# Performance work log

Hardware: AMD Instinct MI355X
Metric: run time of the kernel (lower is better)

## Reference

```python
import jax, jax.numpy as jnp
import numpy as np

SR = 48000
N_FFT = 2048
HOP = 64
N_MELS = 128
N_FREQ = N_FFT // 2 + 1  # 1025
N_TARGETS = 64
BATCH = 32
AUDIO_LEN = SR * 1  # duration = 1 s


def _mel_filterbank():
    # torchaudio melscale_fbanks defaults: htk mel scale, norm=None, f_min=0, f_max=sr/2
    freqs = np.linspace(0.0, SR / 2.0, N_FREQ)
    h2m = lambda f: 2595.0 * np.log10(1.0 + f / 700.0)
    m2h = lambda m: 700.0 * (10.0 ** (m / 2595.0) - 1.0)
    m_pts = np.linspace(h2m(0.0), h2m(SR / 2.0), N_MELS + 2)
    f_pts = m2h(m_pts)
    f_diff = np.diff(f_pts)
    slopes = f_pts[None, :] - freqs[:, None]          # [F, n_mels+2]
    down = -slopes[:, :-2] / f_diff[:-1]
    up = slopes[:, 2:] / f_diff[1:]
    fb = np.maximum(0.0, np.minimum(down, up))        # [F, n_mels]
    return fb.astype(np.float32)


def _mel_spec(x, fb):
    # x: [B, L] raw audio -> [B, n_mels, T] power mel spectrogram (power=2, center=True, hann)
    pad = N_FFT // 2
    xp = jnp.pad(x, ((0, 0), (pad, pad)), mode='reflect')
    n_frames = 1 + x.shape[-1] // HOP                 # 751
    idx = jnp.arange(n_frames)[:, None] * HOP + jnp.arange(N_FFT)[None, :]
    frames = xp[:, idx]                               # [B, T, n_fft]
    win = (0.5 * (1.0 - jnp.cos(2.0 * jnp.pi * jnp.arange(N_FFT) / N_FFT))).astype(x.dtype)
    spec = jnp.fft.rfft(frames * win, axis=-1)        # [B, T, F]
    power = spec.real ** 2 + spec.imag ** 2
    return jnp.einsum('btf,fm->bmt', power, fb)       # [B, n_mels, T]


def setup_inputs() -> dict:
    key = jax.random.key(0)
    k1, k2 = jax.random.split(key)
    fb = jnp.asarray(_mel_filterbank())
    x = jax.random.normal(k1, (BATCH, AUDIO_LEN), dtype=jnp.float32) * 0.1
    target_audio = jax.random.normal(k2, (N_TARGETS, AUDIO_LEN), dtype=jnp.float32) * 0.1
    mel_targets = _mel_spec(target_audio, fb)         # [N, n_mels, T]
    return {"x": x, "mel_targets": mel_targets, "mel_fb": fb}


def reference(x, mel_targets, mel_fb):
    m = _mel_spec(x, mel_fb)                          # [B, n_mels, T]
    # mean abs diff of each candidate vs every target: [B, N]
    diffs = jnp.mean(jnp.abs(m[:, None, :, :] - mel_targets[None, :, :, :]), axis=(-1, -2))
    minimums = jnp.min(diffs, axis=-1)                # [B]
    return (minimums,)
```

## Files before the change

### kernel.cpp

```cpp
#include <hip/hip_runtime.h>
#include <math.h>

#define SRATE   48000
#define NFFT    2048
#define N1      1024
#define HOP     64
#define NMELS   128
#define NFREQ   1025
#define NTGT    64
#define BATCH   32
#define NFRAMES 751
#define MELSZ   (NMELS * NFRAMES)
#define NCHUNK  751
#define CPB     1
#define NB_B    ((NCHUNK + CPB - 1) / CPB)
#define PADW    132

__device__ __forceinline__ int SP(int a) { return a + 5 * (a >> 5); }
#define SBUF1 1179
__device__ __forceinline__ int TP(int a) { return a + (a >> 5); }
#define TWP   263

__global__ __launch_bounds__(256) void tab_kernel(
    float* __restrict__ wtab, float* __restrict__ gtwc, float* __restrict__ gtws) {
  int i = blockIdx.x * 256 + threadIdx.x;
  if (i < NFFT)
    wtab[i] = 0.5f - 0.5f * cosf((float)(2.0 * M_PI / NFFT) * (float)i);
  if (i <= 1024) {
    float sv, cv;
    sincosf(-(float)(2.0 * M_PI / NFFT) * (float)i, &sv, &cv);
    gtwc[i] = cv;
    gtws[i] = sv;
  }
}

__global__ __launch_bounds__(256) void fbt_kernel(
    const float* __restrict__ fb, float* __restrict__ fbT,
    int* __restrict__ fs, int* __restrict__ fe) {
  int m = blockIdx.x;
  int tid = threadIdx.x;
  __shared__ int smin[256], smax[256];
  int lmin = NFREQ, lmax = -1;
  for (int f = tid; f < NFREQ; f += 256) {
    float v = fb[f * NMELS + m];
    fbT[m * NFREQ + f] = v;
    if (v > 0.0f) {
      if (f < lmin) lmin = f;
      if (f > lmax) lmax = f;
    }
  }
  smin[tid] = lmin;
  smax[tid] = lmax;
  __syncthreads();
  for (int off = 128; off > 0; off >>= 1) {
    if (tid < off) {
      smin[tid] = min(smin[tid], smin[tid + off]);
      smax[tid] = max(smax[tid], smax[tid + off]);
    }
    __syncthreads();
  }
  if (tid == 0) {
    fs[m] = smin[0];
    fe[m] = smax[0];
  }
}

template<int L>
__device__ __forceinline__ void r4_1024(
    const float* __restrict__ sre, const float* __restrict__ sim,
    float* __restrict__ dre, float* __restrict__ dim_,
    const float* __restrict__ twc, const float* __restrict__ tws, int t) {
  constexpr int LOG2L = (L == 1) ? 0 : (L == 4) ? 2 : (L == 16) ? 4
                      : (L == 64) ? 6 : 8;
  constexpr int TS = 256 / L;
  int k = t & (L - 1);
  int j = t >> LOG2L;
  int rb = SP(t);
  float u0r = sre[rb],       u0i = sim[rb];
  float u1r = sre[rb + 296], u1i = sim[rb + 296];
  float u2r = sre[rb + 592], u2i = sim[rb + 592];
  float u3r = sre[rb + 888], u3i = sim[rb + 888];
  float a1r, a1i, a2r, a2i, a3r, a3i;
  if (L == 1) {
    a1r = u1r; a1i = u1i; a2r = u2r; a2i = u2i; a3r = u3r; a3i = u3i;
  } else {
    int tp = TP(k * TS);
    float wc1 = twc[tp], ws1 = tws[tp];
    float wc2 = wc1 * wc1 - ws1 * ws1, ws2 = 2.0f * wc1 * ws1;
    float wc3 = wc2 * wc1 - ws2 * ws1, ws3 = wc2 * ws1 + ws2 * wc1;
    a1r = wc1 * u1r - ws1 * u1i; a1i = wc1 * u1i + ws1 * u1r;
    a2r = wc2 * u2r - ws2 * u2i; a2i = wc2 * u2i + ws2 * u2r;
    a3r = wc3 * u3r - ws3 * u3i; a3i = wc3 * u3i + ws3 * u3r;
  }
  float s0r = u0r + a2r, s0i = u0i + a2i;
  float d0r = u0r - a2r, d0i = u0i - a2i;
  float s1r = a1r + a3r, s1i = a1i + a3i;
  float d1r = a1r - a3r, d1i = a1i - a3i;
  int wb = (j << (LOG2L + 2)) + k;
  int o0 = SP(wb), o1 = SP(wb + L), o2 = SP(wb + 2 * L), o3 = SP(wb + 3 * L);
  dre[o0] = s0r + s1r;  dim_[o0] = s0i + s1i;
  dre[o1] = d0r + d1i;  dim_[o1] = d0i - d1r;
  dre[o2] = s0r - s1r;  dim_[o2] = s0i - s1i;
  dre[o3] = d0r - d1i;  dim_[o3] = d0i + d1r;
}

__global__ __launch_bounds__(256) void melspec_kernel(
    const float* __restrict__ x, const float* __restrict__ fbT,
    const int* __restrict__ fs, const int* __restrict__ fe,
    const float* __restrict__ wtab, const float* __restrict__ gtwc,
    const float* __restrict__ gtws, float* __restrict__ mel) {
  __shared__ float lds[4 * SBUF1 + 2 * TWP];
  float* reA  = lds;
  float* imA  = lds + SBUF1;
  float* reB  = lds + 2 * SBUF1;
  float* imB  = lds + 3 * SBUF1;
  float* tw1c = lds + 4 * SBUF1;
  float* tw1s = lds + 4 * SBUF1 + TWP;

  int tid = threadIdx.x;
  int b = blockIdx.x / NFRAMES;
  int t = blockIdx.x - b * NFRAMES;
  const float* xb = x + (size_t)b * SRATE;

  {
    int j = tid;
    tw1c[TP(j)] = gtwc[2 * j];
    tw1s[TP(j)] = gtws[2 * j];
  }
  for (int n = tid; n < N1; n += 256) {
    int i0 = 2 * n, i1 = 2 * n + 1;
    int p0 = t * HOP + i0 - NFFT / 2;
    p0 = p0 < 0 ? -p0 : (p0 >= SRATE ? 2 * SRATE - 2 - p0 : p0);
    int p1 = t * HOP + i1 - NFFT / 2;
    p1 = p1 < 0 ? -p1 : (p1 >= SRATE ? 2 * SRATE - 2 - p1 : p1);
    int s = SP(n);
    reA[s] = xb[p0] * wtab[i0];
    imA[s] = xb[p1] * wtab[i1];
  }
  __syncthreads();

  r4_1024<1>(reA, imA, reB, imB, tw1c, tw1s, tid);   __syncthreads();
  r4_1024<4>(reB, imB, reA, imA, tw1c, tw1s, tid);   __syncthreads();
  r4_1024<16>(reA, imA, reB, imB, tw1c, tw1s, tid);  __syncthreads();
  r4_1024<64>(reB, imB, reA, imA, tw1c, tw1s, tid);  __syncthreads();
  r4_1024<256>(reA, imA, reB, imB, tw1c, tw1s, tid); __syncthreads();

  for (int k = tid; k <= 1024; k += 256) {
    int ka = SP(k & (N1 - 1)), kb = SP((N1 - k) & (N1 - 1));
    float Zar = reB[ka], Zai = imB[ka];
    float Zbr = reB[kb], Zbi = imB[kb];
    float Xer  = 0.5f * (Zar + Zbr), Xei = 0.5f * (Zai - Zbi);
    float Xor_ = 0.5f * (Zai + Zbi), Xoi = 0.5f * (Zbr - Zar);
    float wc = gtwc[k], ws = gtws[k];
    float Xr = Xer + wc * Xor_ - ws * Xoi;
    float Xi = Xei + wc * Xoi + ws * Xor_;
    reA[k] = Xr * Xr + Xi * Xi;
  }
  __syncthreads();

  int m = tid >> 1, half = tid & 1;
  int f0 = fs[m], f1 = fe[m];
  int mid = f0 + ((f1 - f0 + 1) >> 1);
  int lo = half ? mid : f0;
  int hi = half ? f1 : mid - 1;
  const float* col = fbT + (size_t)m * NFREQ;
  float acc = 0.0f;
  for (int f = lo; f <= hi; ++f) acc += reA[f] * col[f];
  acc += __shfl_xor(acc, 1);
  if (!half) mel[(size_t)b * MELSZ + m * NFRAMES + t] = acc;
}

__global__ __launch_bounds__(256) void diff_kernel(
    const float* __restrict__ mel, const float* __restrict__ tgt,
    float* __restrict__ part) {
  __shared__ float mel_s[BATCH * PADW];
  __shared__ float tgt_s[NTGT * PADW];
  int tid = threadIdx.x;
  int b = tid >> 3;
  int kb = tid & 7;

  float acc[8];
  #pragma unroll
  for (int i = 0; i < 8; ++i) acc[i] = 0.0f;

  for (int cc = 0; cc < CPB; ++cc) {
    int c = blockIdx.x * CPB + cc;
    if (c >= NCHUNK) break;
    __syncthreads();
    for (int q = tid; q < BATCH * 32; q += 256) {
      int row = q >> 5, c4 = q & 31;
      float4 v = *(const float4*)(mel + (size_t)row * MELSZ + c * 128 + c4 * 4);
      *(float4*)(&mel_s[row * PADW + c4 * 4]) = v;
    }
    for (int q = tid; q < NTGT * 32; q += 256) {
      int row = q >> 5, c4 = q & 31;
      float4 v = *(const float4*)(tgt + (size_t)row * MELSZ + c * 128 + c4 * 4);
      *(float4*)(&tgt_s[row * PADW + c4 * 4]) = v;
    }
    __syncthreads();
    for (int j4 = 0; j4 < 32; ++j4) {
      float4 mv = *(const float4*)(&mel_s[b * PADW + j4 * 4]);
      #pragma unroll
      for (int i = 0; i < 8; ++i) {
        int k = kb + (i << 3);
        float4 tv = *(const float4*)(&tgt_s[k * PADW + j4 * 4]);
        acc[i] += fabsf(mv.x - tv.x) + fabsf(mv.y - tv.y) +
                  fabsf(mv.z - tv.z) + fabsf(mv.w - tv.w);
      }
    }
  }

  #pragma unroll
  for (int i = 0; i < 8; ++i)
    part[(size_t)blockIdx.x * 2048 + b * 64 + kb + (i << 3)] = acc[i];
}

__global__ __launch_bounds__(256) void reduce_kernel(
    const float* __restrict__ part, float* __restrict__ out) {
  __shared__ float ds[256];
  int tid = threadIdx.x;
  int p = blockIdx.x * 256 + tid;
  float s = 0.0f;
  for (int bb = 0; bb < NB_B; ++bb) s += part[(size_t)bb * 2048 + p];
  ds[tid] = s * (1.0f / (float)MELSZ);
  __syncthreads();
  if (tid < 4) {
    float mn = ds[tid * 64];
    #pragma unroll
    for (int kk = 1; kk < 64; ++kk) mn = fminf(mn, ds[tid * 64 + kk]);
    out[blockIdx.x * 4 + tid] = mn;
  }
}

extern "C" void kernel_launch(void* const* d_in, const int* in_sizes, int n_in,
                              void* d_out, int out_size, void* d_ws, size_t ws_size,
                              hipStream_t stream) {
  const float* x   = (const float*)d_in[0];
  const float* tgt = (const float*)d_in[1];
  const float* fb  = (const float*)d_in[2];
  float* out = (float*)d_out;

  char* ws = (char*)d_ws;
  size_t off = 0;
  float* fbT = (float*)(ws + off);
  off += ((size_t)NMELS * NFREQ * sizeof(float) + 255) & ~(size_t)255;
  int* fs = (int*)(ws + off); off += 1024;
  int* fe = (int*)(ws + off); off += 1024;
  float* wtab = (float*)(ws + off); off += NFFT * sizeof(float);
  float* gtwc = (float*)(ws + off); off += 1056 * sizeof(float);
  float* gtws = (float*)(ws + off); off += 1056 * sizeof(float);
  float* mel = (float*)(ws + off);
  off += (size_t)BATCH * MELSZ * sizeof(float);
  float* part = (float*)(ws + off);
  off += (size_t)NB_B * 2048 * sizeof(float);

  tab_kernel<<<8, 256, 0, stream>>>(wtab, gtwc, gtws);
  fbt_kernel<<<NMELS, 256, 0, stream>>>(fb, fbT, fs, fe);
  melspec_kernel<<<BATCH * NFRAMES, 256, 0, stream>>>(
      x, fbT, fs, fe, wtab, gtwc, gtws, mel);
  diff_kernel<<<NB_B, 256, 0, stream>>>(mel, tgt, part);
  reduce_kernel<<<8, 256, 0, stream>>>(part, out);
}
```

Baseline: 291.3 us.

## Interleave complex FFT data as float2, vectorize frame loads, atomically reduce diffs

The FFT workspace in LDS moves from split real/imag arrays to interleaved float2, and the window and twiddle tables become float2, so each butterfly reads and writes complex values with single 64-bit LDS accesses. Interior frame samples are loaded as float2 from global memory, with the reflect-padding path kept only at the edges. The diff kernel computes a 2x4 register tile per thread and atomically adds into a single 2048-entry buffer. This removes the per-chunk partial buffer and the long serial sum in the reduce kernel, at the cost of many float atomics, a memset launch, and order-dependent float summation.

New measurement: 241.4 us. 17.1% less time.

```diff
diff --git a/kernel.cpp b/kernel.cpp
--- a/kernel.cpp
+++ b/kernel.cpp
@@ -12,8 +12,6 @@
 #define NFRAMES 751
 #define MELSZ   (NMELS * NFRAMES)
 #define NCHUNK  751
-#define CPB     1
-#define NB_B    ((NCHUNK + CPB - 1) / CPB)
 #define PADW    132
 
 __device__ __forceinline__ int SP(int a) { return a + 5 * (a >> 5); }
@@ -22,15 +20,17 @@
 #define TWP   263
 
 __global__ __launch_bounds__(256) void tab_kernel(
-    float* __restrict__ wtab, float* __restrict__ gtwc, float* __restrict__ gtws) {
+    float2* __restrict__ wtab2, float2* __restrict__ gtw) {
   int i = blockIdx.x * 256 + threadIdx.x;
-  if (i < NFFT)
-    wtab[i] = 0.5f - 0.5f * cosf((float)(2.0 * M_PI / NFFT) * (float)i);
+  if (i < N1) {
+    float w0 = 0.5f - 0.5f * cosf((float)(2.0 * M_PI / NFFT) * (float)(2 * i));
+    float w1 = 0.5f - 0.5f * cosf((float)(2.0 * M_PI / NFFT) * (float)(2 * i + 1));
+    wtab2[i] = make_float2(w0, w1);
+  }
   if (i <= 1024) {
     float sv, cv;
     sincosf(-(float)(2.0 * M_PI / NFFT) * (float)i, &sv, &cv);
-    gtwc[i] = cv;
-    gtws[i] = sv;
+    gtw[i] = make_float2(cv, sv);
   }
 }
 
@@ -67,94 +67,87 @@
 
 template<int L>
 __device__ __forceinline__ void r4_1024(
-    const float* __restrict__ sre, const float* __restrict__ sim,
-    float* __restrict__ dre, float* __restrict__ dim_,
-    const float* __restrict__ twc, const float* __restrict__ tws, int t) {
+    const float2* __restrict__ s, float2* __restrict__ d,
+    const float2* __restrict__ tw, int t) {
   constexpr int LOG2L = (L == 1) ? 0 : (L == 4) ? 2 : (L == 16) ? 4
                       : (L == 64) ? 6 : 8;
   constexpr int TS = 256 / L;
   int k = t & (L - 1);
   int j = t >> LOG2L;
   int rb = SP(t);
-  float u0r = sre[rb],       u0i = sim[rb];
-  float u1r = sre[rb + 296], u1i = sim[rb + 296];
-  float u2r = sre[rb + 592], u2i = sim[rb + 592];
-  float u3r = sre[rb + 888], u3i = sim[rb + 888];
+  float2 u0 = s[rb], u1 = s[rb + 296], u2 = s[rb + 592], u3 = s[rb + 888];
   float a1r, a1i, a2r, a2i, a3r, a3i;
   if (L == 1) {
-    a1r = u1r; a1i = u1i; a2r = u2r; a2i = u2i; a3r = u3r; a3i = u3i;
+    a1r = u1.x; a1i = u1.y; a2r = u2.x; a2i = u2.y; a3r = u3.x; a3i = u3.y;
   } else {
-    int tp = TP(k * TS);
-    float wc1 = twc[tp], ws1 = tws[tp];
+    float2 w = tw[TP(k * TS)];
+    float wc1 = w.x, ws1 = w.y;
     float wc2 = wc1 * wc1 - ws1 * ws1, ws2 = 2.0f * wc1 * ws1;
     float wc3 = wc2 * wc1 - ws2 * ws1, ws3 = wc2 * ws1 + ws2 * wc1;
-    a1r = wc1 * u1r - ws1 * u1i; a1i = wc1 * u1i + ws1 * u1r;
-    a2r = wc2 * u2r - ws2 * u2i; a2i = wc2 * u2i + ws2 * u2r;
-    a3r = wc3 * u3r - ws3 * u3i; a3i = wc3 * u3i + ws3 * u3r;
-  }
-  float s0r = u0r + a2r, s0i = u0i + a2i;
-  float d0r = u0r - a2r, d0i = u0i - a2i;
+    a1r = wc1 * u1.x - ws1 * u1.y; a1i = wc1 * u1.y + ws1 * u1.x;
+    a2r = wc2 * u2.x - ws2 * u2.y; a2i = wc2 * u2.y + ws2 * u2.x;
+    a3r = wc3 * u3.x - ws3 * u3.y; a3i = wc3 * u3.y + ws3 * u3.x;
+  }
+  float s0r = u0.x + a2r, s0i = u0.y + a2i;
+  float d0r = u0.x - a2r, d0i = u0.y - a2i;
   float s1r = a1r + a3r, s1i = a1i + a3i;
   float d1r = a1r - a3r, d1i = a1i - a3i;
   int wb = (j << (LOG2L + 2)) + k;
-  int o0 = SP(wb), o1 = SP(wb + L), o2 = SP(wb + 2 * L), o3 = SP(wb + 3 * L);
-  dre[o0] = s0r + s1r;  dim_[o0] = s0i + s1i;
-  dre[o1] = d0r + d1i;  dim_[o1] = d0i - d1r;
-  dre[o2] = s0r - s1r;  dim_[o2] = s0i - s1i;
-  dre[o3] = d0r - d1i;  dim_[o3] = d0i + d1r;
+  d[SP(wb)]         = make_float2(s0r + s1r, s0i + s1i);
+  d[SP(wb + L)]     = make_float2(d0r + d1i, d0i - d1r);
+  d[SP(wb + 2 * L)] = make_float2(s0r - s1r, s0i - s1i);
+  d[SP(wb + 3 * L)] = make_float2(d0r - d1i, d0i + d1r);
 }
 
 __global__ __launch_bounds__(256) void melspec_kernel(
     const float* __restrict__ x, const float* __restrict__ fbT,
     const int* __restrict__ fs, const int* __restrict__ fe,
-    const float* __restrict__ wtab, const float* __restrict__ gtwc,
-    const float* __restrict__ gtws, float* __restrict__ mel) {
-  __shared__ float lds[4 * SBUF1 + 2 * TWP];
-  float* reA  = lds;
-  float* imA  = lds + SBUF1;
-  float* reB  = lds + 2 * SBUF1;
-  float* imB  = lds + 3 * SBUF1;
-  float* tw1c = lds + 4 * SBUF1;
-  float* tw1s = lds + 4 * SBUF1 + TWP;
+    const float2* __restrict__ wtab2, const float2* __restrict__ gtw,
+    float* __restrict__ mel) {
+  __shared__ float2 zA[SBUF1];
+  __shared__ float2 zB[SBUF1];
+  __shared__ float2 twl[TWP];
 
   int tid = threadIdx.x;
   int b = blockIdx.x / NFRAMES;
   int t = blockIdx.x - b * NFRAMES;
   const float* xb = x + (size_t)b * SRATE;
 
-  {
-    int j = tid;
-    tw1c[TP(j)] = gtwc[2 * j];
-    tw1s[TP(j)] = gtws[2 * j];
-  }
+  twl[TP(tid)] = gtw[2 * tid];
+
+  int base = t * HOP - NFFT / 2;
   for (int n = tid; n < N1; n += 256) {
-    int i0 = 2 * n, i1 = 2 * n + 1;
-    int p0 = t * HOP + i0 - NFFT / 2;
-    p0 = p0 < 0 ? -p0 : (p0 >= SRATE ? 2 * SRATE - 2 - p0 : p0);
-    int p1 = t * HOP + i1 - NFFT / 2;
-    p1 = p1 < 0 ? -p1 : (p1 >= SRATE ? 2 * SRATE - 2 - p1 : p1);
-    int s = SP(n);
-    reA[s] = xb[p0] * wtab[i0];
-    imA[s] = xb[p1] * wtab[i1];
-  }
-  __syncthreads();
-
-  r4_1024<1>(reA, imA, reB, imB, tw1c, tw1s, tid);   __syncthreads();
-  r4_1024<4>(reB, imB, reA, imA, tw1c, tw1s, tid);   __syncthreads();
-  r4_1024<16>(reA, imA, reB, imB, tw1c, tw1s, tid);  __syncthreads();
-  r4_1024<64>(reB, imB, reA, imA, tw1c, tw1s, tid);  __syncthreads();
-  r4_1024<256>(reA, imA, reB, imB, tw1c, tw1s, tid); __syncthreads();
-
+    int p0 = base + 2 * n;
+    float2 v;
+    if (p0 >= 0 && p0 + 1 < SRATE) {
+      v = *(const float2*)(xb + p0);
+    } else {
+      int q0 = p0 < 0 ? -p0 : (p0 >= SRATE ? 2 * SRATE - 2 - p0 : p0);
+      int p1 = p0 + 1;
+      int q1 = p1 < 0 ? -p1 : (p1 >= SRATE ? 2 * SRATE - 2 - p1 : p1);
+      v = make_float2(xb[q0], xb[q1]);
+    }
+    float2 w2 = wtab2[n];
+    zA[SP(n)] = make_float2(v.x * w2.x, v.y * w2.y);
+  }
+  __syncthreads();
+
+  r4_1024<1>(zA, zB, twl, tid);   __syncthreads();
+  r4_1024<4>(zB, zA, twl, tid);   __syncthreads();
+  r4_1024<16>(zA, zB, twl, tid);  __syncthreads();
+  r4_1024<64>(zB, zA, twl, tid);  __syncthreads();
+  r4_1024<256>(zA, zB, twl, tid); __syncthreads();
+
+  float* pw = (float*)zA;
   for (int k = tid; k <= 1024; k += 256) {
     int ka = SP(k & (N1 - 1)), kb = SP((N1 - k) & (N1 - 1));
-    float Zar = reB[ka], Zai = imB[ka];
-    float Zbr = reB[kb], Zbi = imB[kb];
-    float Xer  = 0.5f * (Zar + Zbr), Xei = 0.5f * (Zai - Zbi);
-    float Xor_ = 0.5f * (Zai + Zbi), Xoi = 0.5f * (Zbr - Zar);
-    float wc = gtwc[k], ws = gtws[k];
-    float Xr = Xer + wc * Xor_ - ws * Xoi;
-    float Xi = Xei + wc * Xoi + ws * Xor_;
-    reA[k] = Xr * Xr + Xi * Xi;
+    float2 Za = zB[ka], Zb = zB[kb];
+    float Xer  = 0.5f * (Za.x + Zb.x), Xei = 0.5f * (Za.y - Zb.y);
+    float Xor_ = 0.5f * (Za.y + Zb.y), Xoi = 0.5f * (Zb.x - Za.x);
+    float2 w = gtw[k];
+    float Xr = Xer + w.x * Xor_ - w.y * Xoi;
+    float Xi = Xei + w.x * Xoi + w.y * Xor_;
+    pw[k] = Xr * Xr + Xi * Xi;
   }
   __syncthreads();
 
@@ -165,64 +158,66 @@
   int hi = half ? f1 : mid - 1;
   const float* col = fbT + (size_t)m * NFREQ;
   float acc = 0.0f;
-  for (int f = lo; f <= hi; ++f) acc += reA[f] * col[f];
+  for (int f = lo; f <= hi; ++f) acc += pw[f] * col[f];
   acc += __shfl_xor(acc, 1);
   if (!half) mel[(size_t)b * MELSZ + m * NFRAMES + t] = acc;
 }
 
 __global__ __launch_bounds__(256) void diff_kernel(
     const float* __restrict__ mel, const float* __restrict__ tgt,
-    float* __restrict__ part) {
+    float* __restrict__ diffs) {
   __shared__ float mel_s[BATCH * PADW];
   __shared__ float tgt_s[NTGT * PADW];
   int tid = threadIdx.x;
-  int b = tid >> 3;
-  int kb = tid & 7;
-
-  float acc[8];
+  int bg = tid >> 4;
+  int kg = tid & 15;
+  int c = blockIdx.x;
+
+  for (int q = tid; q < BATCH * 32; q += 256) {
+    int row = q >> 5, c4 = q & 31;
+    float4 v = *(const float4*)(mel + (size_t)row * MELSZ + c * 128 + c4 * 4);
+    *(float4*)(&mel_s[row * PADW + c4 * 4]) = v;
+  }
+  for (int q = tid; q < NTGT * 32; q += 256) {
+    int row = q >> 5, c4 = q & 31;
+    float4 v = *(const float4*)(tgt + (size_t)row * MELSZ + c * 128 + c4 * 4);
+    *(float4*)(&tgt_s[row * PADW + c4 * 4]) = v;
+  }
+  __syncthreads();
+
+  float acc[2][4];
   #pragma unroll
-  for (int i = 0; i < 8; ++i) acc[i] = 0.0f;
-
-  for (int cc = 0; cc < CPB; ++cc) {
-    int c = blockIdx.x * CPB + cc;
-    if (c >= NCHUNK) break;
-    __syncthreads();
-    for (int q = tid; q < BATCH * 32; q += 256) {
-      int row = q >> 5, c4 = q & 31;
-      float4 v = *(const float4*)(mel + (size_t)row * MELSZ + c * 128 + c4 * 4);
-      *(float4*)(&mel_s[row * PADW + c4 * 4]) = v;
-    }
-    for (int q = tid; q < NTGT * 32; q += 256) {
-      int row = q >> 5, c4 = q & 31;
-      float4 v = *(const float4*)(tgt + (size_t)row * MELSZ + c * 128 + c4 * 4);
-      *(float4*)(&tgt_s[row * PADW + c4 * 4]) = v;
-    }
-    __syncthreads();
-    for (int j4 = 0; j4 < 32; ++j4) {
-      float4 mv = *(const float4*)(&mel_s[b * PADW + j4 * 4]);
-      #pragma unroll
-      for (int i = 0; i < 8; ++i) {
-        int k = kb + (i << 3);
-        float4 tv = *(const float4*)(&tgt_s[k * PADW + j4 * 4]);
-        acc[i] += fabsf(mv.x - tv.x) + fabsf(mv.y - tv.y) +
-                  fabsf(mv.z - tv.z) + fabsf(mv.w - tv.w);
-      }
+  for (int bi = 0; bi < 2; ++bi)
+    #pragma unroll
+    for (int i = 0; i < 4; ++i) acc[bi][i] = 0.0f;
+
+  for (int j4 = 0; j4 < 32; ++j4) {
+    float4 m0 = *(const float4*)(&mel_s[(2 * bg) * PADW + j4 * 4]);
+    float4 m1 = *(const float4*)(&mel_s[(2 * bg + 1) * PADW + j4 * 4]);
+    #pragma unroll
+    for (int i = 0; i < 4; ++i) {
+      int k = kg + (i << 4);
+      float4 tv = *(const float4*)(&tgt_s[k * PADW + j4 * 4]);
+      acc[0][i] += fabsf(m0.x - tv.x) + fabsf(m0.y - tv.y) +
+                   fabsf(m0.z - tv.z) + fabsf(m0.w - tv.w);
+      acc[1][i] += fabsf(m1.x - tv.x) + fabsf(m1.y - tv.y) +
+                   fabsf(m1.z - tv.z) + fabsf(m1.w - tv.w);
     }
   }
 
   #pragma unroll
-  for (int i = 0; i < 8; ++i)
-    part[(size_t)blockIdx.x * 2048 + b * 64 + kb + (i << 3)] = acc[i];
+  for (int bi = 0; bi < 2; ++bi)
+    #pragma unroll
+    for (int i = 0; i < 4; ++i)
+      atomicAdd(&diffs[(2 * bg + bi) * 64 + kg + (i << 4)], acc[bi][i]);
 }
 
 __global__ __launch_bounds__(256) void reduce_kernel(
-    const float* __restrict__ part, float* __restrict__ out) {
+    const float* __restrict__ diffs, float* __restrict__ out) {
   __shared__ float ds[256];
   int tid = threadIdx.x;
   int p = blockIdx.x * 256 + tid;
-  float s = 0.0f;
-  for (int bb = 0; bb < NB_B; ++bb) s += part[(size_t)bb * 2048 + p];
-  ds[tid] = s * (1.0f / (float)MELSZ);
+  ds[tid] = diffs[p] * (1.0f / (float)MELSZ);
   __syncthreads();
   if (tid < 4) {
     float mn = ds[tid * 64];
@@ -246,18 +241,17 @@
   off += ((size_t)NMELS * NFREQ * sizeof(float) + 255) & ~(size_t)255;
   int* fs = (int*)(ws + off); off += 1024;
   int* fe = (int*)(ws + off); off += 1024;
-  float* wtab = (float*)(ws + off); off += NFFT * sizeof(float);
-  float* gtwc = (float*)(ws + off); off += 1056 * sizeof(float);
-  float* gtws = (float*)(ws + off); off += 1056 * sizeof(float);
+  float2* wtab2 = (float2*)(ws + off); off += N1 * sizeof(float2);
+  float2* gtw   = (float2*)(ws + off); off += 1056 * sizeof(float2);
   float* mel = (float*)(ws + off);
   off += (size_t)BATCH * MELSZ * sizeof(float);
-  float* part = (float*)(ws + off);
-  off += (size_t)NB_B * 2048 * sizeof(float);
-
-  tab_kernel<<<8, 256, 0, stream>>>(wtab, gtwc, gtws);
+  float* diffs = (float*)(ws + off); off += 2048 * sizeof(float);
+
+  hipMemsetAsync(diffs, 0, 2048 * sizeof(float), stream);
+  tab_kernel<<<8, 256, 0, stream>>>(wtab2, gtw);
   fbt_kernel<<<NMELS, 256, 0, stream>>>(fb, fbT, fs, fe);
   melspec_kernel<<<BATCH * NFRAMES, 256, 0, stream>>>(
-      x, fbT, fs, fe, wtab, gtwc, gtws, mel);
-  diff_kernel<<<NB_B, 256, 0, stream>>>(mel, tgt, part);
-  reduce_kernel<<<8, 256, 0, stream>>>(part, out);
-}
+      x, fbT, fs, fe, wtab2, gtw, mel);
+  diff_kernel<<<NCHUNK, 256, 0, stream>>>(mel, tgt, diffs);
+  reduce_kernel<<<8, 256, 0, stream>>>(diffs, out);
+}
```
